# Performance work log

Hardware: AMD Instinct MI355X
Metric: run time of the kernel (lower is better)

Reference implementation:

```python
import jax, jax.numpy as jnp
import numpy as np

SIGMA = 1.0
RADIUS = 4  # skimage.filters.gaussian: truncate=4.0 -> radius=int(4.0*1.0+0.5)=4 (9 taps)
NBINS = 256  # skimage.filters.threshold_otsu default


def _gauss_kernel(dtype):
    x = jnp.arange(-RADIUS, RADIUS + 1, dtype=dtype)
    k = jnp.exp(-0.5 * (x / SIGMA) ** 2)
    return k / k.sum()


def _blur(img):
    # img: [B, H, W]; separable Gaussian, 'nearest' (edge) boundary like scipy/skimage.
    k = _gauss_kernel(img.dtype)
    p = jnp.pad(img, ((0, 0), (RADIUS, RADIUS), (0, 0)), mode='edge')
    out = jax.lax.conv_general_dilated(p[:, None], k.reshape(1, 1, 2 * RADIUS + 1, 1),
                                       (1, 1), 'VALID')[:, 0]
    p = jnp.pad(out, ((0, 0), (0, 0), (RADIUS, RADIUS)), mode='edge')
    out = jax.lax.conv_general_dilated(p[:, None], k.reshape(1, 1, 1, 2 * RADIUS + 1),
                                       (1, 1), 'VALID')[:, 0]
    return out


def _otsu(img):
    # img: [H, W] -> scalar Otsu threshold (256-bin histogram over [min, max]).
    lo, hi = img.min(), img.max()
    width = (hi - lo) / NBINS
    idx = jnp.clip(jnp.floor((img - lo) / jnp.maximum(width, 1e-12)).astype(jnp.int32),
                   0, NBINS - 1)
    counts = jnp.zeros(NBINS, img.dtype).at[idx.ravel()].add(1.0)
    centers = lo + (jnp.arange(NBINS, dtype=img.dtype) + 0.5) * width
    w1 = jnp.cumsum(counts)                      # class-0 weight
    w2 = jnp.cumsum(counts[::-1])[::-1]          # class-1 weight
    cs = jnp.cumsum(counts * centers)
    rcs = jnp.cumsum((counts * centers)[::-1])[::-1]
    m1 = cs / jnp.maximum(w1, 1e-12)
    m2 = rcs / jnp.maximum(w2, 1e-12)
    var12 = w1[:-1] * w2[1:] * (m1[:-1] - m2[1:]) ** 2
    return centers[jnp.argmax(var12)]


def reference(x):
    # x: [B, 4, H, W]; channel 0 = thermal (normalized mean=std=0.5), last 3 = RGB.
    thermal = jnp.clip(x[:, 0] * 0.5 + 0.5, 0.0, 1.0)          # denormalize [B,H,W]
    blurred = _blur(thermal)
    t = jax.vmap(_otsu)(blurred)                               # [B]
    mask = jnp.where(blurred > t[:, None, None], 1.0, blurred)  # soft alpha mask
    rgb = x[:, -3:]                                            # [B,3,H,W]
    alpha = mask[:, None]                                      # [B,1,H,W]
    # skimage rgba2rgb with white background: clip(alpha*rgb + (1-alpha)*1)
    return jnp.clip(alpha * rgb + (1.0 - alpha), 0.0, 1.0)


def setup_inputs() -> dict:
    key = jax.random.key(0)
    x = jax.random.normal(key, (32, 4, 512, 512), dtype=jnp.float32)
    return {"x": x}
```

## Files before the change

### kernel.cpp

```cpp
#include <hip/hip_runtime.h>
#include <math.h>

#pragma clang fp contract(off)

struct GaussW { float w[9]; };

__global__ __launch_bounds__(256) void init_kernel(unsigned* __restrict__ hist,
                                                   unsigned* __restrict__ minmax, int nimg) {
    #pragma clang fp contract(off)
    int i = blockIdx.x * 256 + threadIdx.x;
    if (i < nimg * 256) hist[i] = 0u;
    if (i < nimg) { minmax[2 * i] = 0x7F800000u; minmax[2 * i + 1] = 0u; }
}

__global__ __launch_bounds__(256) void blur_kernel(const float* __restrict__ x,
                                                   float* __restrict__ blurred,
                                                   unsigned* __restrict__ minmax, GaussW gw) {
    #pragma clang fp contract(off)
    __shared__ float s_in[72][72];
    __shared__ float s_vb[64][72];
    const int tid = threadIdx.x;
    const int b = blockIdx.z;
    const int r0 = blockIdx.y * 64, c0 = blockIdx.x * 64;
    const float* img0 = x + (size_t)b * 4 * 262144;

    for (int i = tid; i < 72 * 72; i += 256) {
        int r = i / 72, c = i - r * 72;
        int gr = min(max(r0 + r - 4, 0), 511);
        int gc = min(max(c0 + c - 4, 0), 511);
        float v = img0[gr * 512 + gc];
        s_in[r][c] = fminf(fmaxf(v * 0.5f + 0.5f, 0.0f), 1.0f);
    }
    __syncthreads();
    for (int i = tid; i < 64 * 72; i += 256) {
        int r = i / 72, c = i - r * 72;
        float q0 = s_in[r + 0][c] * gw.w[0];
        float q1 = s_in[r + 1][c] * gw.w[1];
        float q2 = s_in[r + 2][c] * gw.w[2];
        float q3 = s_in[r + 3][c] * gw.w[3];
        float q4 = s_in[r + 4][c] * gw.w[4];
        float q5 = s_in[r + 5][c] * gw.w[5];
        float q6 = s_in[r + 6][c] * gw.w[6];
        float q7 = s_in[r + 7][c] * gw.w[7];
        float q8 = s_in[r + 8][c] * gw.w[8];
        float acc = ((q0 + q1) + (q2 + q3)) + ((q4 + q5) + (q6 + q7));
        acc = acc + q8;
        s_vb[r][c] = acc;
    }
    __syncthreads();
    float lmin = 1e30f, lmax = -1e30f;
    float* bimg = blurred + (size_t)b * 262144;
    for (int i = tid; i < 64 * 64; i += 256) {
        int r = i >> 6, c = i & 63;
        float q0 = s_vb[r][c + 0] * gw.w[0];
        float q1 = s_vb[r][c + 1] * gw.w[1];
        float q2 = s_vb[r][c + 2] * gw.w[2];
        float q3 = s_vb[r][c + 3] * gw.w[3];
        float q4 = s_vb[r][c + 4] * gw.w[4];
        float q5 = s_vb[r][c + 5] * gw.w[5];
        float q6 = s_vb[r][c + 6] * gw.w[6];
        float q7 = s_vb[r][c + 7] * gw.w[7];
        float q8 = s_vb[r][c + 8] * gw.w[8];
        float acc = ((q0 + q1) + (q2 + q3)) + ((q4 + q5) + (q6 + q7));
        acc = acc + q8;
        bimg[(r0 + r) * 512 + (c0 + c)] = acc;
        lmin = fminf(lmin, acc);
        lmax = fmaxf(lmax, acc);
    }
    for (int off = 32; off >= 1; off >>= 1) {
        lmin = fminf(lmin, __shfl_down(lmin, off));
        lmax = fmaxf(lmax, __shfl_down(lmax, off));
    }
    __shared__ float smin[4], smax[4];
    int wave = tid >> 6, lane = tid & 63;
    if (lane == 0) { smin[wave] = lmin; smax[wave] = lmax; }
    __syncthreads();
    if (tid == 0) {
        float mn = fminf(fminf(smin[0], smin[1]), fminf(smin[2], smin[3]));
        float mx = fmaxf(fmaxf(smax[0], smax[1]), fmaxf(smax[2], smax[3]));
        atomicMin(&minmax[2 * b], __float_as_uint(mn));
        atomicMax(&minmax[2 * b + 1], __float_as_uint(mx));
    }
}

__global__ __launch_bounds__(256) void hist_kernel(const float* __restrict__ blurred,
                                                   const unsigned* __restrict__ minmax,
                                                   unsigned* __restrict__ hist) {
    #pragma clang fp contract(off)
    const int b = blockIdx.y;
    __shared__ unsigned sh[256];
    sh[threadIdx.x] = 0u;
    __syncthreads();
    const float lo = __uint_as_float(minmax[2 * b]);
    const float hi = __uint_as_float(minmax[2 * b + 1]);
    const float width = (hi - lo) * 0.00390625f;
    const float denom = fmaxf(width, 1e-12f);
    const float4* img = (const float4*)(blurred + (size_t)b * 262144);
    for (int i = blockIdx.x * blockDim.x + threadIdx.x; i < 65536; i += gridDim.x * blockDim.x) {
        float4 v = img[i];
        int i0 = min(max((int)floorf((v.x - lo) / denom), 0), 255);
        int i1 = min(max((int)floorf((v.y - lo) / denom), 0), 255);
        int i2 = min(max((int)floorf((v.z - lo) / denom), 0), 255);
        int i3 = min(max((int)floorf((v.w - lo) / denom), 0), 255);
        atomicAdd(&sh[i0], 1u);
        atomicAdd(&sh[i1], 1u);
        atomicAdd(&sh[i2], 1u);
        atomicAdd(&sh[i3], 1u);
    }
    __syncthreads();
    atomicAdd(&hist[b * 256 + threadIdx.x], sh[threadIdx.x]);
}

__global__ __launch_bounds__(256) void otsu_kernel(const unsigned* __restrict__ hist,
                                                   const unsigned* __restrict__ minmax,
                                                   float* __restrict__ t) {
    #pragma clang fp contract(off)
    __shared__ float counts[256], centers[256], w1[256], w2[256], cs[256], rcs[256];
    const int b = blockIdx.x, tid = threadIdx.x;
    const float lo = __uint_as_float(minmax[2 * b]);
    const float hi = __uint_as_float(minmax[2 * b + 1]);
    const float width = (hi - lo) * 0.00390625f;
    counts[tid] = (float)hist[b * 256 + tid];
    centers[tid] = lo + ((float)tid + 0.5f) * width;
    __syncthreads();
    if (tid == 0) {
        float a = 0.f;
        for (int i = 0; i < 256; ++i) { a = a + counts[i]; w1[i] = a; }
        a = 0.f;
        for (int i = 255; i >= 0; --i) { a = a + counts[i]; w2[i] = a; }
        a = 0.f;
        for (int i = 0; i < 256; ++i) { a = a + counts[i] * centers[i]; cs[i] = a; }
        a = 0.f;
        for (int i = 255; i >= 0; --i) { a = a + counts[i] * centers[i]; rcs[i] = a; }
        float best = -1e30f; int bi = 0;
        for (int i = 0; i < 255; ++i) {
            float m1 = cs[i] / fmaxf(w1[i], 1e-12f);
            float m2 = rcs[i + 1] / fmaxf(w2[i + 1], 1e-12f);
            float d = m1 - m2;
            float v = (w1[i] * w2[i + 1]) * (d * d);
            if (v > best) { best = v; bi = i; }
        }
        t[b] = centers[bi];
    }
}

__global__ __launch_bounds__(256) void final_kernel(const float* __restrict__ x,
                                                    const float* __restrict__ blurred,
                                                    const float* __restrict__ tarr,
                                                    float* __restrict__ out, int total4) {
    #pragma clang fp contract(off)
    int i = blockIdx.x * 256 + threadIdx.x;
    if (i >= total4) return;
    int b = i >> 16;
    int p = i & 65535;
    float tb = tarr[b];
    float4 bl = ((const float4*)(blurred + (size_t)b * 262144))[p];
    float4 m;
    m.x = (bl.x > tb) ? 1.0f : bl.x;
    m.y = (bl.y > tb) ? 1.0f : bl.y;
    m.z = (bl.z > tb) ? 1.0f : bl.z;
    m.w = (bl.w > tb) ? 1.0f : bl.w;
    const float4* xim = (const float4*)(x + (size_t)b * 4 * 262144);
    float4* oim = (float4*)(out + (size_t)b * 3 * 262144);
#pragma unroll
    for (int c = 0; c < 3; ++c) {
        float4 rgb = xim[(size_t)(c + 1) * 65536 + p];
        float4 o;
        o.x = fminf(fmaxf(m.x * rgb.x + (1.0f - m.x), 0.f), 1.f);
        o.y = fminf(fmaxf(m.y * rgb.y + (1.0f - m.y), 0.f), 1.f);
        o.z = fminf(fmaxf(m.z * rgb.z + (1.0f - m.z), 0.f), 1.f);
        o.w = fminf(fmaxf(m.w * rgb.w + (1.0f - m.w), 0.f), 1.f);
        oim[(size_t)c * 65536 + p] = o;
    }
}

extern "C" void kernel_launch(void* const* d_in, const int* in_sizes, int n_in,
                              void* d_out, int out_size, void* d_ws, size_t ws_size,
                              hipStream_t stream) {
    const float* x = (const float*)d_in[0];
    float* out = (float*)d_out;
    const int nimg = in_sizes[0] / (4 * 262144);

    float* blurred = (float*)d_ws;
    unsigned* hist = (unsigned*)((char*)d_ws + (size_t)nimg * 262144 * 4);
    unsigned* minmax = hist + (size_t)nimg * 256;
    float* t = (float*)(minmax + (size_t)nimg * 2);

    GaussW gw;
    float kk[9];
    for (int i = 0; i < 9; ++i) {
        double d = (double)(i - 4);
        kk[i] = (float)exp(-0.5 * d * d);
    }
    float s = ((kk[0] + kk[1]) + (kk[2] + kk[3])) + ((kk[4] + kk[5]) + (kk[6] + kk[7]));
    s = s + kk[8];
    for (int i = 0; i < 9; ++i) gw.w[i] = kk[i] / s;

    init_kernel<<<(nimg * 256 + 255) / 256, 256, 0, stream>>>(hist, minmax, nimg);
    dim3 bgrid(8, 8, nimg);
    blur_kernel<<<bgrid, 256, 0, stream>>>(x, blurred, minmax, gw);
    dim3 hgrid(64, nimg);
    hist_kernel<<<hgrid, 256, 0, stream>>>(blurred, minmax, hist);
    otsu_kernel<<<nimg, 256, 0, stream>>>(hist, minmax, t);
    int total4 = nimg * 65536;
    final_kernel<<<(total4 + 255) / 256, 256, 0, stream>>>(x, blurred, t, out, total4);
}
```

Before: 311.2 us.

## Drop init kernel, use per-block partial min/max, parallelize Otsu scans

Removes the init kernel: the histogram is now zeroed inside the blur kernel, and global min/max atomics are replaced by per-tile partial min/max arrays that the hist and otsu kernels reduce with wave shuffles. The hist grid shrinks from 64 to 16 blocks per image, and blocks skip the global atomic for empty bins. The Otsu kernel runs its four prefix scans on four waves in parallel and does the argmax with a wave reduction instead of a single thread. This trims launch overhead and serial tail latency, at the cost of a redundant min/max reduction in two kernels and fewer hist blocks per image.

After: 257.8 us. 1.21x faster.

```diff
diff --git a/kernel.cpp b/kernel.cpp
--- a/kernel.cpp
+++ b/kernel.cpp
@@ -5,23 +5,18 @@
 
 struct GaussW { float w[9]; };
 
-__global__ __launch_bounds__(256) void init_kernel(unsigned* __restrict__ hist,
-                                                   unsigned* __restrict__ minmax, int nimg) {
-    #pragma clang fp contract(off)
-    int i = blockIdx.x * 256 + threadIdx.x;
-    if (i < nimg * 256) hist[i] = 0u;
-    if (i < nimg) { minmax[2 * i] = 0x7F800000u; minmax[2 * i + 1] = 0u; }
-}
-
 __global__ __launch_bounds__(256) void blur_kernel(const float* __restrict__ x,
                                                    float* __restrict__ blurred,
-                                                   unsigned* __restrict__ minmax, GaussW gw) {
+                                                   float* __restrict__ pmin,
+                                                   float* __restrict__ pmax,
+                                                   unsigned* __restrict__ hist, GaussW gw) {
     #pragma clang fp contract(off)
     __shared__ float s_in[72][72];
     __shared__ float s_vb[64][72];
     const int tid = threadIdx.x;
     const int b = blockIdx.z;
     const int r0 = blockIdx.y * 64, c0 = blockIdx.x * 64;
+    if (blockIdx.x == 0 && blockIdx.y == 0) hist[b * 256 + tid] = 0u;
     const float* img0 = x + (size_t)b * 4 * 262144;
 
     for (int i = tid; i < 72 * 72; i += 256) {
@@ -78,25 +73,37 @@
     if (tid == 0) {
         float mn = fminf(fminf(smin[0], smin[1]), fminf(smin[2], smin[3]));
         float mx = fmaxf(fmaxf(smax[0], smax[1]), fmaxf(smax[2], smax[3]));
-        atomicMin(&minmax[2 * b], __float_as_uint(mn));
-        atomicMax(&minmax[2 * b + 1], __float_as_uint(mx));
+        int bid = blockIdx.y * 8 + blockIdx.x;
+        pmin[b * 64 + bid] = mn;
+        pmax[b * 64 + bid] = mx;
     }
 }
 
 __global__ __launch_bounds__(256) void hist_kernel(const float* __restrict__ blurred,
-                                                   const unsigned* __restrict__ minmax,
+                                                   const float* __restrict__ pmin,
+                                                   const float* __restrict__ pmax,
                                                    unsigned* __restrict__ hist) {
     #pragma clang fp contract(off)
     const int b = blockIdx.y;
     __shared__ unsigned sh[256];
+    __shared__ float s_lo, s_hi;
     sh[threadIdx.x] = 0u;
-    __syncthreads();
-    const float lo = __uint_as_float(minmax[2 * b]);
-    const float hi = __uint_as_float(minmax[2 * b + 1]);
+    int wv = threadIdx.x >> 6, ln = threadIdx.x & 63;
+    if (wv == 0) {
+        float v = pmin[b * 64 + ln];
+        for (int off = 32; off >= 1; off >>= 1) v = fminf(v, __shfl_down(v, off));
+        if (ln == 0) s_lo = v;
+    } else if (wv == 1) {
+        float v = pmax[b * 64 + ln];
+        for (int off = 32; off >= 1; off >>= 1) v = fmaxf(v, __shfl_down(v, off));
+        if (ln == 0) s_hi = v;
+    }
+    __syncthreads();
+    const float lo = s_lo, hi = s_hi;
     const float width = (hi - lo) * 0.00390625f;
     const float denom = fmaxf(width, 1e-12f);
     const float4* img = (const float4*)(blurred + (size_t)b * 262144);
-    for (int i = blockIdx.x * blockDim.x + threadIdx.x; i < 65536; i += gridDim.x * blockDim.x) {
+    for (int i = blockIdx.x * 256 + threadIdx.x; i < 65536; i += gridDim.x * 256) {
         float4 v = img[i];
         int i0 = min(max((int)floorf((v.x - lo) / denom), 0), 255);
         int i1 = min(max((int)floorf((v.y - lo) / denom), 0), 255);
@@ -108,39 +115,101 @@
         atomicAdd(&sh[i3], 1u);
     }
     __syncthreads();
-    atomicAdd(&hist[b * 256 + threadIdx.x], sh[threadIdx.x]);
+    unsigned cnt = sh[threadIdx.x];
+    if (cnt) atomicAdd(&hist[b * 256 + threadIdx.x], cnt);
 }
 
 __global__ __launch_bounds__(256) void otsu_kernel(const unsigned* __restrict__ hist,
-                                                   const unsigned* __restrict__ minmax,
+                                                   const float* __restrict__ pmin,
+                                                   const float* __restrict__ pmax,
                                                    float* __restrict__ t) {
     #pragma clang fp contract(off)
     __shared__ float counts[256], centers[256], w1[256], w2[256], cs[256], rcs[256];
+    __shared__ float s_lo, s_hi;
     const int b = blockIdx.x, tid = threadIdx.x;
-    const float lo = __uint_as_float(minmax[2 * b]);
-    const float hi = __uint_as_float(minmax[2 * b + 1]);
+    const int wv = tid >> 6, ln = tid & 63;
+    if (wv == 0) {
+        float v = pmin[b * 64 + ln];
+        for (int off = 32; off >= 1; off >>= 1) v = fminf(v, __shfl_down(v, off));
+        if (ln == 0) s_lo = v;
+    } else if (wv == 1) {
+        float v = pmax[b * 64 + ln];
+        for (int off = 32; off >= 1; off >>= 1) v = fmaxf(v, __shfl_down(v, off));
+        if (ln == 0) s_hi = v;
+    }
+    __syncthreads();
+    const float lo = s_lo, hi = s_hi;
     const float width = (hi - lo) * 0.00390625f;
     counts[tid] = (float)hist[b * 256 + tid];
     centers[tid] = lo + ((float)tid + 0.5f) * width;
     __syncthreads();
-    if (tid == 0) {
-        float a = 0.f;
-        for (int i = 0; i < 256; ++i) { a = a + counts[i]; w1[i] = a; }
-        a = 0.f;
-        for (int i = 255; i >= 0; --i) { a = a + counts[i]; w2[i] = a; }
-        a = 0.f;
-        for (int i = 0; i < 256; ++i) { a = a + counts[i] * centers[i]; cs[i] = a; }
-        a = 0.f;
-        for (int i = 255; i >= 0; --i) { a = a + counts[i] * centers[i]; rcs[i] = a; }
-        float best = -1e30f; int bi = 0;
-        for (int i = 0; i < 255; ++i) {
-            float m1 = cs[i] / fmaxf(w1[i], 1e-12f);
-            float m2 = rcs[i + 1] / fmaxf(w2[i + 1], 1e-12f);
-            float d = m1 - m2;
-            float v = (w1[i] * w2[i + 1]) * (d * d);
-            if (v > best) { best = v; bi = i; }
+    if (ln == 0) {
+        if (wv == 0) {
+            float a = 0.f;
+            for (int i0 = 0; i0 < 256; i0 += 8) {
+                float c0 = counts[i0+0], c1 = counts[i0+1], c2 = counts[i0+2], c3 = counts[i0+3];
+                float c4 = counts[i0+4], c5 = counts[i0+5], c6 = counts[i0+6], c7 = counts[i0+7];
+                a = a + c0; w1[i0+0] = a; a = a + c1; w1[i0+1] = a;
+                a = a + c2; w1[i0+2] = a; a = a + c3; w1[i0+3] = a;
+                a = a + c4; w1[i0+4] = a; a = a + c5; w1[i0+5] = a;
+                a = a + c6; w1[i0+6] = a; a = a + c7; w1[i0+7] = a;
+            }
+        } else if (wv == 1) {
+            float a = 0.f;
+            for (int i0 = 255; i0 >= 7; i0 -= 8) {
+                float c0 = counts[i0-0], c1 = counts[i0-1], c2 = counts[i0-2], c3 = counts[i0-3];
+                float c4 = counts[i0-4], c5 = counts[i0-5], c6 = counts[i0-6], c7 = counts[i0-7];
+                a = a + c0; w2[i0-0] = a; a = a + c1; w2[i0-1] = a;
+                a = a + c2; w2[i0-2] = a; a = a + c3; w2[i0-3] = a;
+                a = a + c4; w2[i0-4] = a; a = a + c5; w2[i0-5] = a;
+                a = a + c6; w2[i0-6] = a; a = a + c7; w2[i0-7] = a;
+            }
+        } else if (wv == 2) {
+            float a = 0.f;
+            for (int i0 = 0; i0 < 256; i0 += 8) {
+                float q0 = counts[i0+0] * centers[i0+0], q1 = counts[i0+1] * centers[i0+1];
+                float q2 = counts[i0+2] * centers[i0+2], q3 = counts[i0+3] * centers[i0+3];
+                float q4 = counts[i0+4] * centers[i0+4], q5 = counts[i0+5] * centers[i0+5];
+                float q6 = counts[i0+6] * centers[i0+6], q7 = counts[i0+7] * centers[i0+7];
+                a = a + q0; cs[i0+0] = a; a = a + q1; cs[i0+1] = a;
+                a = a + q2; cs[i0+2] = a; a = a + q3; cs[i0+3] = a;
+                a = a + q4; cs[i0+4] = a; a = a + q5; cs[i0+5] = a;
+                a = a + q6; cs[i0+6] = a; a = a + q7; cs[i0+7] = a;
+            }
+        } else {
+            float a = 0.f;
+            for (int i0 = 255; i0 >= 7; i0 -= 8) {
+                float q0 = counts[i0-0] * centers[i0-0], q1 = counts[i0-1] * centers[i0-1];
+                float q2 = counts[i0-2] * centers[i0-2], q3 = counts[i0-3] * centers[i0-3];
+                float q4 = counts[i0-4] * centers[i0-4], q5 = counts[i0-5] * centers[i0-5];
+                float q6 = counts[i0-6] * centers[i0-6], q7 = counts[i0-7] * centers[i0-7];
+                a = a + q0; rcs[i0-0] = a; a = a + q1; rcs[i0-1] = a;
+                a = a + q2; rcs[i0-2] = a; a = a + q3; rcs[i0-3] = a;
+                a = a + q4; rcs[i0-4] = a; a = a + q5; rcs[i0-5] = a;
+                a = a + q6; rcs[i0-6] = a; a = a + q7; rcs[i0-7] = a;
+            }
         }
-        t[b] = centers[bi];
+    }
+    __syncthreads();
+    if (wv == 0) {
+        float best = -1e30f; int bi = 0x7fffffff;
+#pragma unroll
+        for (int k = 0; k < 4; ++k) {
+            int i = ln + 64 * k;
+            if (i < 255) {
+                float m1 = cs[i] / fmaxf(w1[i], 1e-12f);
+                float m2 = rcs[i + 1] / fmaxf(w2[i + 1], 1e-12f);
+                float d = m1 - m2;
+                float v = (w1[i] * w2[i + 1]) * (d * d);
+                if (v > best) { best = v; bi = i; }
+            }
+        }
+        for (int off = 32; off >= 1; off >>= 1) {
+            float ov = __shfl_down(best, off);
+            int   oi = __shfl_down(bi, off);
+            if (ov > best || (ov == best && oi < bi)) { best = ov; bi = oi; }
+        }
+        if (ln == 0) t[b] = centers[bi];
     }
 }
 
@@ -182,9 +251,10 @@
     const int nimg = in_sizes[0] / (4 * 262144);
 
     float* blurred = (float*)d_ws;
-    unsigned* hist = (unsigned*)((char*)d_ws + (size_t)nimg * 262144 * 4);
-    unsigned* minmax = hist + (size_t)nimg * 256;
-    float* t = (float*)(minmax + (size_t)nimg * 2);
+    unsigned* hist = (unsigned*)(blurred + (size_t)nimg * 262144);
+    float* pmin = (float*)(hist + (size_t)nimg * 256);
+    float* pmax = pmin + (size_t)nimg * 64;
+    float* t = pmax + (size_t)nimg * 64;
 
     GaussW gw;
     float kk[9];
@@ -196,12 +266,11 @@
     s = s + kk[8];
     for (int i = 0; i < 9; ++i) gw.w[i] = kk[i] / s;
 
-    init_kernel<<<(nimg * 256 + 255) / 256, 256, 0, stream>>>(hist, minmax, nimg);
     dim3 bgrid(8, 8, nimg);
-    blur_kernel<<<bgrid, 256, 0, stream>>>(x, blurred, minmax, gw);
-    dim3 hgrid(64, nimg);
-    hist_kernel<<<hgrid, 256, 0, stream>>>(blurred, minmax, hist);
-    otsu_kernel<<<nimg, 256, 0, stream>>>(hist, minmax, t);
+    blur_kernel<<<bgrid, 256, 0, stream>>>(x, blurred, pmin, pmax, hist, gw);
+    dim3 hgrid(16, nimg);
+    hist_kernel<<<hgrid, 256, 0, stream>>>(blurred, pmin, pmax, hist);
+    otsu_kernel<<<nimg, 256, 0, stream>>>(hist, pmin, pmax, t);
     int total4 = nimg * 65536;
     final_kernel<<<(total4 + 255) / 256, 256, 0, stream>>>(x, blurred, t, out, total4);
 }
```
